# Performance work log

Hardware: AMD Instinct MI355X
Metric: run time of the kernel (lower is better)

Reference implementation:

```python
import jax, jax.numpy as jnp
import numpy as np

N_WORD, N_TOPIC, N_DOC = 50000, 2000, 50000
D_WORD, D_TOPIC, D_OUT = 256, 128, 128
E_WW, E_WT, E_WD, E_TD, E_TT = 500000, 400000, 500000, 400000, 300000


def setup_inputs() -> dict:
    key = jax.random.key(0)
    ks = jax.random.split(key, 32)
    i = iter(range(32))

    def randn(shape, scale=1.0):
        return jax.random.normal(ks[next(i)], shape, dtype=jnp.float32) * scale

    def edges(n_e, n_src, n_dst):
        src = jax.random.randint(ks[next(i)], (n_e,), 0, n_src, dtype=jnp.int32)
        dst = jax.random.randint(ks[next(i)], (n_e,), 0, n_dst, dtype=jnp.int32)
        w = jax.random.uniform(ks[next(i)], (n_e,), dtype=jnp.float32)
        return src, dst, w

    feat_word = randn((N_WORD, D_WORD))
    feat_topic = randn((N_TOPIC, D_TOPIC))
    ww_src, ww_dst, ww_w = edges(E_WW, N_WORD, N_WORD)
    wt_src, wt_dst, wt_w = edges(E_WT, N_WORD, N_TOPIC)
    wd_src, wd_dst, wd_w = edges(E_WD, N_WORD, N_DOC)
    td_src, td_dst, td_w = edges(E_TD, N_TOPIC, N_DOC)
    tt_src, tt_dst, tt_w = edges(E_TT, N_TOPIC, N_TOPIC)
    return dict(
        feat_word=feat_word, feat_topic=feat_topic,
        ww_src=ww_src, ww_dst=ww_dst, ww_w=ww_w,
        wt_src=wt_src, wt_dst=wt_dst, wt_w=wt_w,
        wd_src=wd_src, wd_dst=wd_dst, wd_w=wd_w,
        td_src=td_src, td_dst=td_dst, td_w=td_w,
        tt_src=tt_src, tt_dst=tt_dst, tt_w=tt_w,
        W_ww=randn((D_WORD, D_OUT), 0.02), b_ww=randn((D_OUT,), 0.02),
        W_wt=randn((D_WORD, D_OUT), 0.02), b_wt=randn((D_OUT,), 0.02),
        W_wd=randn((D_WORD, D_OUT), 0.02), b_wd=randn((D_OUT,), 0.02),
        W_td=randn((D_TOPIC, D_OUT), 0.02), b_td=randn((D_OUT,), 0.02),
        W_tt=randn((D_TOPIC, D_OUT), 0.02), b_tt=randn((D_OUT,), 0.02),
    )


def _mean_agg(Wh, src, dst, w, n_dst):
    # u_mul_e: gather src feature, scale by edge weight; fn.mean: divide by in-degree
    m = Wh[src] * w[:, None]                                   # [E, D_OUT]
    s = jax.ops.segment_sum(m, dst, num_segments=n_dst)        # [n_dst, D_OUT]
    deg = jax.ops.segment_sum(jnp.ones_like(w), dst, num_segments=n_dst)
    return jnp.where(deg[:, None] > 0, s / jnp.maximum(deg, 1.0)[:, None], 0.0)


def reference(feat_word, feat_topic,
              ww_src, ww_dst, ww_w, wt_src, wt_dst, wt_w,
              wd_src, wd_dst, wd_w, td_src, td_dst, td_w,
              tt_src, tt_dst, tt_w,
              W_ww, b_ww, W_wt, b_wt, W_wd, b_wd, W_td, b_td, W_tt, b_tt):
    # Per-relation projections (note: in the torch source the causal/noise
    # branches are overwritten by the plain Linear, so this is the effective math).
    Wh_ww = feat_word @ W_ww + b_ww
    Wh_wt = feat_word @ W_wt + b_wt
    Wh_wd = feat_word @ W_wd + b_wd
    Wh_td = feat_topic @ W_td + b_td
    Wh_tt = feat_topic @ W_tt + b_tt
    # mean per edge type, then cross-etype 'sum' per destination node type
    h_word = _mean_agg(Wh_ww, ww_src, ww_dst, ww_w, N_WORD)
    h_topic = (_mean_agg(Wh_wt, wt_src, wt_dst, wt_w, N_TOPIC)
               + _mean_agg(Wh_tt, tt_src, tt_dst, tt_w, N_TOPIC))
    h_doc = (_mean_agg(Wh_wd, wd_src, wd_dst, wd_w, N_DOC)
             + _mean_agg(Wh_td, td_src, td_dst, td_w, N_DOC))
    return h_word, h_topic, h_doc
```

## Files before the change

### kernel.cpp

```cpp
#include <hip/hip_runtime.h>

typedef short short8 __attribute__((ext_vector_type(8)));
typedef float floatx4 __attribute__((ext_vector_type(4)));

__device__ __forceinline__ float b2f(unsigned int u16) {
    union { unsigned int i; float f; } v;
    v.i = u16 << 16;
    return v.f;
}
__device__ __forceinline__ unsigned short f2b(float f) {
    unsigned int i = __float_as_uint(f);
    unsigned int r = (i + 0x7FFFu + ((i >> 16) & 1u)) >> 16;
    return (unsigned short)r;
}

#define N_WORD  50000
#define N_TOPIC 2000
#define N_DOC   50000
#define E_MAX   500000
#define CHAIN_END 0xFFFFFFFFu
#define NB_GEMM 814
#define NSLOT_WW 200000
#define NSLOT_WT 8000
#define NSLOT_TT 8000
#define NSLOT_WD 200000
#define NSLOT_TD 200000
#define NSLOT_ALL (NSLOT_WW + NSLOT_WT + NSLOT_TT + NSLOT_WD + NSLOT_TD)

__global__ void detect_kernel(const unsigned int* __restrict__ feat_u32,
                              unsigned int* __restrict__ flag)
{
    int cnt = 0;
    for (int i = 0; i < 256; ++i) {
        unsigned int u = feat_u32[i];
        int e = (u >> 7) & 0xFF;
        if (e >= 110 && e <= 140) ++cnt;
    }
    *flag = (cnt > 128) ? 1u : 0u;
}

__global__ __launch_bounds__(256) void swizzle_kernel(
    const void* __restrict__ W0, const void* __restrict__ W1,
    const void* __restrict__ W2, const void* __restrict__ W3,
    const void* __restrict__ W4,
    const void* __restrict__ b0, const void* __restrict__ b1,
    const void* __restrict__ b2, const void* __restrict__ b3,
    const void* __restrict__ b4,
    short8* __restrict__ D0, short8* __restrict__ D1,
    short8* __restrict__ D2, short8* __restrict__ D3,
    short8* __restrict__ D4,
    unsigned short* __restrict__ bias_out,
    const unsigned int* __restrict__ flag_p)
{
    const int w = blockIdx.y;
    const void* W; const void* bs; short8* D; int S;
    switch (w) {
        case 0: W = W0; bs = b0; D = D0; S = 8; break;
        case 1: W = W1; bs = b1; D = D1; S = 8; break;
        case 2: W = W2; bs = b2; D = D2; S = 8; break;
        case 3: W = W3; bs = b3; D = D3; S = 4; break;
        default: W = W4; bs = b4; D = D4; S = 4; break;
    }
    const int n_entries = S * 8 * 64;
    const int mode = (int)*flag_p;
    for (int e = blockIdx.x * 256 + threadIdx.x; e < n_entries; e += 8 * 256) {
        const int lane = e & 63, t = (e >> 6) & 7, s = e >> 9;
        const int q = lane >> 4, n = t * 16 + (lane & 15);
        short8 val;
#pragma unroll
        for (int j = 0; j < 8; ++j) {
            const int k = s * 32 + q * 8 + j;
            unsigned short hv = mode ? ((const unsigned short*)W)[k * 128 + n]
                                     : f2b(((const float*)W)[k * 128 + n]);
            val[j] = (short)hv;
        }
        D[e] = val;
    }
    if (blockIdx.x == 0 && threadIdx.x < 128) {
        bias_out[w * 128 + threadIdx.x] =
            mode ? ((const unsigned short*)bs)[threadIdx.x]
                 : f2b(((const float*)bs)[threadIdx.x]);
    }
}

template <int S, int NP>
__device__ __forceinline__ void gemm_body_lds(
    short8* __restrict__ Blds,
    const void* feat_, int n_rows, int bx,
    const short8* Ba, const short8* Bb, const short8* Bc,
    const unsigned short* bias_all, int ba, int bb, int bc,
    unsigned short* Oa, unsigned short* Ob, unsigned short* Oc,
    int mode_bf16)
{
    const int tid = threadIdx.x;
    const int lane = tid & 63;
    const int wave = tid >> 6;
    const int row0 = (bx * 4 + wave) * 16;
    const int m = lane & 15, q = lane >> 4;
    const int K = S * 32;
    int arow_idx = row0 + m;
    if (arow_idx >= n_rows) arow_idx = n_rows - 1;

    short8 a[S];
    if (mode_bf16) {
        const short8* arow = (const short8*)((const unsigned short*)feat_ + (size_t)arow_idx * K);
#pragma unroll
        for (int s = 0; s < S; ++s) a[s] = arow[s * 4 + q];
    } else {
        const float* arow = (const float*)feat_ + (size_t)arow_idx * K;
#pragma unroll
        for (int s = 0; s < S; ++s) {
            const float4 f0 = ((const float4*)arow)[s * 8 + q * 2];
            const float4 f1 = ((const float4*)arow)[s * 8 + q * 2 + 1];
            short8 t;
            t[0] = (short)f2b(f0.x); t[1] = (short)f2b(f0.y);
            t[2] = (short)f2b(f0.z); t[3] = (short)f2b(f0.w);
            t[4] = (short)f2b(f1.x); t[5] = (short)f2b(f1.y);
            t[6] = (short)f2b(f1.z); t[7] = (short)f2b(f1.w);
            a[s] = t;
        }
    }

    constexpr int NH = (S * 8 * 64 > 2048) ? 2 : 1;
    constexpr int SH = S / NH;

#pragma unroll
    for (int p = 0; p < NP; ++p) {
        const short8* B = (p == 0) ? Ba : ((p == 1) ? Bb : Bc);
        const unsigned short* bias = bias_all + ((p == 0) ? ba : ((p == 1) ? bb : bc)) * 128;
        unsigned short* O = (p == 0) ? Oa : ((p == 1) ? Ob : Oc);

        floatx4 acc[8];
#pragma unroll
        for (int t = 0; t < 8; ++t) { acc[t][0] = 0.f; acc[t][1] = 0.f; acc[t][2] = 0.f; acc[t][3] = 0.f; }

#pragma unroll
        for (int h = 0; h < NH; ++h) {
            __syncthreads();
            for (int i = tid; i < SH * 8 * 64; i += 256) Blds[i] = B[h * (SH * 8 * 64) + i];
            __syncthreads();
#pragma unroll
            for (int s = 0; s < SH; ++s) {
#pragma unroll
                for (int t = 0; t < 8; ++t) {
                    short8 b = Blds[(s * 8 + t) * 64 + lane];
                    acc[t] = __builtin_amdgcn_mfma_f32_16x16x32_bf16(a[h * SH + s], b, acc[t], 0, 0, 0);
                }
            }
        }

#pragma unroll
        for (int t = 0; t < 8; ++t) {
            const float bb_ = b2f((unsigned int)bias[t * 16 + m]);
#pragma unroll
            for (int r = 0; r < 4; ++r) {
                const int row = row0 + q * 4 + r;
                if (row < n_rows)
                    O[(size_t)row * 128 + t * 16 + m] = f2b(acc[t][r] + bb_);
            }
        }
    }
}

__global__ __launch_bounds__(256) void link_gemm_kernel(
    const void* __restrict__ feat_word, const void* __restrict__ feat_topic,
    const short8* __restrict__ Bww, const short8* __restrict__ Bwt,
    const short8* __restrict__ Bwd, const short8* __restrict__ Btt,
    const short8* __restrict__ Btd,
    const unsigned short* __restrict__ bias_all,
    unsigned short* __restrict__ Wh_ww, unsigned short* __restrict__ Wh_wt,
    unsigned short* __restrict__ Wh_wd, unsigned short* __restrict__ Wh_tt,
    unsigned short* __restrict__ Wh_td,
    const int* s0, const int* d0, const void* w0, int n0, unsigned int* h0, unsigned long long* e0,
    const int* s1, const int* d1, const void* w1, int n1, unsigned int* h1, unsigned long long* e1,
    const int* s2, const int* d2, const void* w2, int n2, unsigned int* h2, unsigned long long* e2,
    const int* s3, const int* d3, const void* w3, int n3, unsigned int* h3, unsigned long long* e3,
    const int* s4, const int* d4, const void* w4, int n4, unsigned int* h4, unsigned long long* e4,
    const unsigned int* __restrict__ flag_p)
{
    __shared__ short8 Blds[2048];
    const int mode = (int)*flag_p;

    if (blockIdx.x < NB_GEMM) {
        if (blockIdx.x < 782) {
            gemm_body_lds<8, 3>(Blds, feat_word, N_WORD, blockIdx.x, Bww, Bwt, Bwd,
                                bias_all, 0, 1, 2, Wh_ww, Wh_wt, Wh_wd, mode);
        } else {
            gemm_body_lds<4, 2>(Blds, feat_topic, N_TOPIC, blockIdx.x - 782, Btt, Btd,
                                (const short8*)nullptr, bias_all, 4, 3, 0,
                                Wh_tt, Wh_td, (unsigned short*)nullptr, mode);
        }
        return;
    }

    int lb = blockIdx.x - NB_GEMM;
    const int nb0 = (n0 + 255) >> 8, nb1 = (n1 + 255) >> 8, nb2 = (n2 + 255) >> 8,
              nb3 = (n3 + 255) >> 8;
    const int* src; const int* dst; const void* w_; int n;
    unsigned int* head; unsigned long long* ent;
    if (lb < nb0)      { src = s0; dst = d0; w_ = w0; n = n0; head = h0; ent = e0; }
    else if ((lb -= nb0) < nb1) { src = s1; dst = d1; w_ = w1; n = n1; head = h1; ent = e1; }
    else if ((lb -= nb1) < nb2) { src = s2; dst = d2; w_ = w2; n = n2; head = h2; ent = e2; }
    else if ((lb -= nb2) < nb3) { src = s3; dst = d3; w_ = w3; n = n3; head = h3; ent = e3; }
    else { lb -= nb3;  src = s4; dst = d4; w_ = w4; n = n4; head = h4; ent = e4; }

    const int i = lb * 256 + threadIdx.x;
    if (i >= n) return;
    const int d = dst[i];
    const unsigned int slot = (unsigned int)d * 4 + ((unsigned int)i & 3);
    const unsigned int old = atomicExch(&head[slot], (unsigned int)i);
    const unsigned short w16 = mode ? ((const unsigned short*)w_)[i]
                                    : f2b(((const float*)w_)[i]);
    ent[i] = ((unsigned long long)old << 32)
           | ((unsigned long long)w16 << 16)
           | (unsigned long long)(unsigned int)src[i];
}

__device__ __forceinline__ void acc8(float a[8], const uint4& u, float w)
{
    a[0] += b2f(u.x & 0xffffu) * w; a[1] += b2f(u.x >> 16) * w;
    a[2] += b2f(u.y & 0xffffu) * w; a[3] += b2f(u.y >> 16) * w;
    a[4] += b2f(u.z & 0xffffu) * w; a[5] += b2f(u.z >> 16) * w;
    a[6] += b2f(u.w & 0xffffu) * w; a[7] += b2f(u.w >> 16) * w;
}

__device__ __forceinline__ void walk1(
    const unsigned long long* __restrict__ ent,
    const unsigned short* __restrict__ Wh,
    unsigned int e, int sl, float a[8], float& cnt)
{
    bool live = (e != CHAIN_END);
    unsigned long long v = ent[live ? e : 0];
    while (live) {
        const unsigned int nx = (unsigned int)(v >> 32);
        const bool live_n = (nx != CHAIN_END);
        const unsigned long long vn = ent[live_n ? nx : 0];
        const uint4 u = ((const uint4*)(Wh + (size_t)((unsigned int)v & 0xffffu) * 128))[sl];
        acc8(a, u, b2f(((unsigned int)v) >> 16));
        cnt += 1.0f;
        v = vn; live = live_n;
    }
}

__device__ __forceinline__ void walk2(
    const unsigned long long* __restrict__ ent1, const unsigned short* __restrict__ Wh1, unsigned int e1,
    const unsigned long long* __restrict__ ent2, const unsigned short* __restrict__ Wh2, unsigned int e2,
    int sl, float a1[8], float a2[8], float& c1, float& c2)
{
    bool l1 = (e1 != CHAIN_END), l2 = (e2 != CHAIN_END);
    unsigned long long v1 = ent1[l1 ? e1 : 0];
    unsigned long long v2 = ent2[l2 ? e2 : 0];
    while (l1 || l2) {
        const unsigned int n1 = (unsigned int)(v1 >> 32);
        const unsigned int n2 = (unsigned int)(v2 >> 32);
        const bool l1n = l1 && (n1 != CHAIN_END);
        const bool l2n = l2 && (n2 != CHAIN_END);
        const unsigned long long v1n = ent1[l1n ? n1 : 0];
        const unsigned long long v2n = ent2[l2n ? n2 : 0];
        const uint4 u1 = ((const uint4*)(Wh1 + (size_t)((unsigned int)v1 & 0xffffu) * 128))[sl];
        const uint4 u2 = ((const uint4*)(Wh2 + (size_t)((unsigned int)v2 & 0xffffu) * 128))[sl];
        if (l1) { acc8(a1, u1, b2f(((unsigned int)v1) >> 16)); c1 += 1.0f; }
        if (l2) { acc8(a2, u2, b2f(((unsigned int)v2) >> 16)); c2 += 1.0f; }
        v1 = v1n; v2 = v2n; l1 = l1n; l2 = l2n;
    }
}

__device__ __forceinline__ void write8(
    void* out, size_t off_elems, int node, int sl, const float r[8], int mode)
{
    if (mode) {
        uint4 o;
        o.x = (unsigned int)f2b(r[0]) | ((unsigned int)f2b(r[1]) << 16);
        o.y = (unsigned int)f2b(r[2]) | ((unsigned int)f2b(r[3]) << 16);
        o.z = (unsigned int)f2b(r[4]) | ((unsigned int)f2b(r[5]) << 16);
        o.w = (unsigned int)f2b(r[6]) | ((unsigned int)f2b(r[7]) << 16);
        *(uint4*)((unsigned short*)out + off_elems + (size_t)node * 128 + sl * 8) = o;
    } else {
        float* p = (float*)out + off_elems + (size_t)node * 128 + sl * 8;
        ((float4*)p)[0] = make_float4(r[0], r[1], r[2], r[3]);
        ((float4*)p)[1] = make_float4(r[4], r[5], r[6], r[7]);
    }
}

__device__ __forceinline__ void dual_body(
    const unsigned int* __restrict__ h1, const unsigned long long* __restrict__ e1t,
    const unsigned short* __restrict__ Wh1,
    const unsigned int* __restrict__ h2, const unsigned long long* __restrict__ e2t,
    const unsigned short* __restrict__ Wh2,
    void* __restrict__ out, size_t off_elems, int blk, int mode)
{
    const int sl = threadIdx.x & 15;
    const int grp = (threadIdx.x >> 4) & 3;
    const int wave = threadIdx.x >> 6;
    const int node = blk * 4 + wave;
    float a1[8] = {0,0,0,0,0,0,0,0}, a2[8] = {0,0,0,0,0,0,0,0};
    float c1 = 0.f, c2 = 0.f;
    walk2(e1t, Wh1, h1[node * 4 + grp], e2t, Wh2, h2[node * 4 + grp],
          sl, a1, a2, c1, c2);
#pragma unroll
    for (int j = 0; j < 8; ++j) {
        a1[j] += __shfl_xor(a1[j], 16); a1[j] += __shfl_xor(a1[j], 32);
        a2[j] += __shfl_xor(a2[j], 16); a2[j] += __shfl_xor(a2[j], 32);
    }
    c1 += __shfl_xor(c1, 16); c1 += __shfl_xor(c1, 32);
    c2 += __shfl_xor(c2, 16); c2 += __shfl_xor(c2, 32);
    const float i1 = (c1 > 0.f) ? 1.f / c1 : 0.f;
    const float i2 = (c2 > 0.f) ? 1.f / c2 : 0.f;
    float r[8];
#pragma unroll
    for (int j = 0; j < 8; ++j) r[j] = a1[j] * i1 + a2[j] * i2;
    if (grp == 0) write8(out, off_elems, node, sl, r, mode);
}

__device__ __forceinline__ void word_body(
    const unsigned int* __restrict__ h_ww, const unsigned long long* __restrict__ e_ww,
    const unsigned short* __restrict__ Wh_ww,
    void* __restrict__ out, int blk, int mode)
{
    const int sl = threadIdx.x & 15;
    const int grp = (threadIdx.x >> 4) & 3;
    const int wave = threadIdx.x >> 6;
    const int node = blk * 4 + wave;
    float a[8] = {0,0,0,0,0,0,0,0}; float cnt = 0.f;
    walk1(e_ww, Wh_ww, h_ww[node * 4 + grp], sl, a, cnt);
#pragma unroll
    for (int j = 0; j < 8; ++j) { a[j] += __shfl_xor(a[j], 16); a[j] += __shfl_xor(a[j], 32); }
    cnt += __shfl_xor(cnt, 16); cnt += __shfl_xor(cnt, 32);
    const float inv = (cnt > 0.f) ? 1.f / cnt : 0.f;
    float r[8];
#pragma unroll
    for (int j = 0; j < 8; ++j) r[j] = a[j] * inv;
    if (grp == 0) write8(out, 0, node, sl, r, mode);
}

__global__ __launch_bounds__(256) void gather_all_kernel(
    const unsigned int* __restrict__ h_wt, const unsigned long long* __restrict__ e_wt,
    const unsigned short* __restrict__ Wh_wt,
    const unsigned int* __restrict__ h_tt, const unsigned long long* __restrict__ e_tt,
    const unsigned short* __restrict__ Wh_tt,
    const unsigned int* __restrict__ h_wd, const unsigned long long* __restrict__ e_wd,
    const unsigned short* __restrict__ Wh_wd,
    const unsigned int* __restrict__ h_td, const unsigned long long* __restrict__ e_td,
    const unsigned short* __restrict__ Wh_td,
    const unsigned int* __restrict__ h_ww, const unsigned long long* __restrict__ e_ww,
    const unsigned short* __restrict__ Wh_ww,
    void* __restrict__ out,
    const unsigned int* __restrict__ flag_p)
{
    const int mode = (int)*flag_p;
    if (blockIdx.x < 500) {
        dual_body(h_wt, e_wt, Wh_wt, h_tt, e_tt, Wh_tt,
                  out, (size_t)6400000, blockIdx.x, mode);
    } else if (blockIdx.x < 13000) {
        dual_body(h_wd, e_wd, Wh_wd, h_td, e_td, Wh_td,
                  out, (size_t)6656000, blockIdx.x - 500, mode);
    } else {
        word_body(h_ww, e_ww, Wh_ww, out, blockIdx.x - 13000, mode);
    }
}

__global__ __launch_bounds__(256) void gather_dt_kernel(
    const unsigned int* __restrict__ h_wt, const unsigned long long* __restrict__ e_wt,
    const unsigned short* __restrict__ Wh_wt,
    const unsigned int* __restrict__ h_tt, const unsigned long long* __restrict__ e_tt,
    const unsigned short* __restrict__ Wh_tt,
    const unsigned int* __restrict__ h_wd, const unsigned long long* __restrict__ e_wd,
    const unsigned short* __restrict__ Wh_wd,
    const unsigned int* __restrict__ h_td, const unsigned long long* __restrict__ e_td,
    const unsigned short* __restrict__ Wh_td,
    void* __restrict__ out,
    const unsigned int* __restrict__ flag_p)
{
    const int mode = (int)*flag_p;
    if (blockIdx.x < 500) {
        dual_body(h_wt, e_wt, Wh_wt, h_tt, e_tt, Wh_tt,
                  out, (size_t)6400000, blockIdx.x, mode);
    } else {
        dual_body(h_wd, e_wd, Wh_wd, h_td, e_td, Wh_td,
                  out, (size_t)6656000, blockIdx.x - 500, mode);
    }
}

__global__ __launch_bounds__(256) void gather_w_kernel(
    const unsigned int* __restrict__ h_ww, const unsigned long long* __restrict__ e_ww,
    const unsigned short* __restrict__ Wh_ww,
    void* __restrict__ out,
    const unsigned int* __restrict__ flag_p)
{
    word_body(h_ww, e_ww, Wh_ww, out, blockIdx.x, (int)*flag_p);
}

extern "C" void kernel_launch(void* const* d_in, const int* in_sizes, int n_in,
                              void* d_out, int out_size, void* d_ws, size_t ws_size,
                              hipStream_t stream)
{
    const void* feat_word  = d_in[0];
    const void* feat_topic = d_in[1];
    const int* ww_src = (const int*)d_in[2];
    const int* ww_dst = (const int*)d_in[3];
    const void* ww_w = d_in[4];
    const int* wt_src = (const int*)d_in[5];
    const int* wt_dst = (const int*)d_in[6];
    const void* wt_w = d_in[7];
    const int* wd_src = (const int*)d_in[8];
    const int* wd_dst = (const int*)d_in[9];
    const void* wd_w = d_in[10];
    const int* td_src = (const int*)d_in[11];
    const int* td_dst = (const int*)d_in[12];
    const void* td_w = d_in[13];
    const int* tt_src = (const int*)d_in[14];
    const int* tt_dst = (const int*)d_in[15];
    const void* tt_w = d_in[16];
    const void* W_ww = d_in[17];
    const void* b_ww = d_in[18];
    const void* W_wt = d_in[19];
    const void* b_wt = d_in[20];
    const void* W_wd = d_in[21];
    const void* b_wd = d_in[22];
    const void* W_td = d_in[23];
    const void* b_td = d_in[24];
    const void* W_tt = d_in[25];
    const void* b_tt = d_in[26];

    const int E_ww = in_sizes[2];
    const int E_wt = in_sizes[5];
    const int E_wd = in_sizes[8];
    const int E_td = in_sizes[11];
    const int E_tt = in_sizes[14];

    char* ws = (char*)d_ws;
    unsigned int* flag = (unsigned int*)ws;
    unsigned int* head_base = (unsigned int*)(ws + 4);
    unsigned int* h_ww = head_base;
    unsigned int* h_wt = h_ww + NSLOT_WW;
    unsigned int* h_tt = h_wt + NSLOT_WT;
    unsigned int* h_wd = h_tt + NSLOT_TT;
    unsigned int* h_td = h_wd + NSLOT_WD;
    size_t off = 4 + (size_t)NSLOT_ALL * 4;
    off = (off + 15) & ~(size_t)15;
    short8* Bsw_ww = (short8*)(ws + off); off += 65536;
    short8* Bsw_wt = (short8*)(ws + off); off += 65536;
    short8* Bsw_wd = (short8*)(ws + off); off += 65536;
    short8* Bsw_td = (short8*)(ws + off); off += 32768;
    short8* Bsw_tt = (short8*)(ws + off); off += 32768;
    unsigned short* bias_all = (unsigned short*)(ws + off); off += 5 * 128 * 2;
    off = (off + 15) & ~(size_t)15;
    unsigned short* Wh_ww = (unsigned short*)(ws + off); off += (size_t)N_WORD * 128 * 2;
    unsigned short* Wh_wt = (unsigned short*)(ws + off); off += (size_t)N_WORD * 128 * 2;
    unsigned short* Wh_tt = (unsigned short*)(ws + off); off += (size_t)N_TOPIC * 128 * 2;
    unsigned short* Wh_td = (unsigned short*)(ws + off); off += (size_t)N_TOPIC * 128 * 2;
    off = (off + 7) & ~(size_t)7;
    unsigned long long* e_ww = (unsigned long long*)(ws + off); off += (size_t)E_MAX * 8;
    unsigned long long* e_wt = (unsigned long long*)(ws + off); off += (size_t)E_MAX * 8;
    unsigned long long* e_tt = (unsigned long long*)(ws + off); off += (size_t)E_MAX * 8;
    unsigned long long* e_wd = (unsigned long long*)(ws + off); off += (size_t)E_MAX * 8;
    unsigned long long* e_td = (unsigned long long*)(ws + off); off += (size_t)E_MAX * 8;

    off = (off + 15) & ~(size_t)15;
    const size_t whwd_bytes = (size_t)N_WORD * 128 * 2;
    const bool fuse_gather = (ws_size >= off + whwd_bytes);
    unsigned short* Wh_wd = fuse_gather ? (unsigned short*)(ws + off)
                                        : (unsigned short*)d_out;

    detect_kernel<<<1, 1, 0, stream>>>((const unsigned int*)feat_word, flag);
    hipMemsetAsync(head_base, 0xFF, (size_t)NSLOT_ALL * 4, stream);

    swizzle_kernel<<<dim3(8, 5), 256, 0, stream>>>(
        W_ww, W_wt, W_wd, W_td, W_tt, b_ww, b_wt, b_wd, b_td, b_tt,
        Bsw_ww, Bsw_wt, Bsw_wd, Bsw_td, Bsw_tt, bias_all, flag);

    const int nb_link = ((E_ww + 255) / 256) + ((E_wt + 255) / 256) +
                        ((E_tt + 255) / 256) + ((E_wd + 255) / 256) +
                        ((E_td + 255) / 256);
    link_gemm_kernel<<<NB_GEMM + nb_link, 256, 0, stream>>>(
        feat_word, feat_topic, Bsw_ww, Bsw_wt, Bsw_wd, Bsw_tt, Bsw_td,
        bias_all, Wh_ww, Wh_wt, Wh_wd, Wh_tt, Wh_td,
        ww_src, ww_dst, ww_w, E_ww, h_ww, e_ww,
        wt_src, wt_dst, wt_w, E_wt, h_wt, e_wt,
        tt_src, tt_dst, tt_w, E_tt, h_tt, e_tt,
        wd_src, wd_dst, wd_w, E_wd, h_wd, e_wd,
        td_src, td_dst, td_w, E_td, h_td, e_td, flag);

    if (fuse_gather) {
        gather_all_kernel<<<500 + 12500 + 12500, 256, 0, stream>>>(
            h_wt, e_wt, Wh_wt, h_tt, e_tt, Wh_tt,
            h_wd, e_wd, Wh_wd, h_td, e_td, Wh_td,
            h_ww, e_ww, Wh_ww, d_out, flag);
    } else {
        gather_dt_kernel<<<500 + 12500, 256, 0, stream>>>(
            h_wt, e_wt, Wh_wt, h_tt, e_tt, Wh_tt,
            h_wd, e_wd, Wh_wd, h_td, e_td, Wh_td, d_out, flag);
        gather_w_kernel<<<12500, 256, 0, stream>>>(
            h_ww, e_ww, Wh_ww, d_out, flag);
    }
}
```

Measured before the change: 381.1 us.

## Replace linked-list edge chains with per-destination fixed-capacity slabs plus overflow lists

For the word-word, word-doc and topic-doc relations, edges are now bucketed into per-destination slabs of capacity C using an atomic counter, with a linked-list overflow chain for nodes whose degree exceeds C. The gather kernels read payloads contiguously and issue up to four row loads at once, instead of chasing dependent pointers through 4-way split chains. Each node is now handled by a 16-lane group rather than a full wave. The aim is to cut the serial latency of pointer chasing in the gather. The trade-offs are contended atomicAdd on counters, slab capacity sized from leftover workspace, and always using the unfused two-kernel gather path with Wh_wd placed in the output buffer.

```diff
diff --git a/kernel.cpp b/kernel.cpp
--- a/kernel.cpp
+++ b/kernel.cpp
@@ -17,15 +17,11 @@
 #define N_WORD  50000
 #define N_TOPIC 2000
 #define N_DOC   50000
-#define E_MAX   500000
 #define CHAIN_END 0xFFFFFFFFu
 #define NB_GEMM 814
-#define NSLOT_WW 200000
-#define NSLOT_WT 8000
-#define NSLOT_TT 8000
-#define NSLOT_WD 200000
-#define NSLOT_TD 200000
-#define NSLOT_ALL (NSLOT_WW + NSLOT_WT + NSLOT_TT + NSLOT_WD + NSLOT_TD)
+#define NPAD    50048
+#define NSLOT_WT (N_TOPIC * 4)
+#define NSLOT_TT (N_TOPIC * 4)
 
 __global__ void detect_kernel(const unsigned int* __restrict__ feat_u32,
                               unsigned int* __restrict__ flag)
@@ -162,6 +158,26 @@
     }
 }
 
+__device__ __forceinline__ void link_slab(
+    const int* __restrict__ src, const int* __restrict__ dst,
+    const void* __restrict__ w_, int n, int i, int mode, int C,
+    unsigned int* __restrict__ cnt, unsigned int* __restrict__ ohead,
+    unsigned long long* __restrict__ oent, unsigned int* __restrict__ slab)
+{
+    if (i >= n) return;
+    const int d = dst[i];
+    const unsigned short w16 = mode ? ((const unsigned short*)w_)[i]
+                                    : f2b(((const float*)w_)[i]);
+    const unsigned int pay = ((unsigned int)w16 << 16) | (unsigned int)src[i];
+    const unsigned int pos = atomicAdd(&cnt[d], 1u);
+    if (pos < (unsigned int)C) {
+        slab[(size_t)d * C + pos] = pay;
+    } else {
+        const unsigned int old = atomicExch(&ohead[d], (unsigned int)i);
+        oent[i] = ((unsigned long long)old << 32) | (unsigned long long)pay;
+    }
+}
+
 __global__ __launch_bounds__(256) void link_gemm_kernel(
     const void* __restrict__ feat_word, const void* __restrict__ feat_topic,
     const short8* __restrict__ Bww, const short8* __restrict__ Bwt,
@@ -171,11 +187,15 @@
     unsigned short* __restrict__ Wh_ww, unsigned short* __restrict__ Wh_wt,
     unsigned short* __restrict__ Wh_wd, unsigned short* __restrict__ Wh_tt,
     unsigned short* __restrict__ Wh_td,
-    const int* s0, const int* d0, const void* w0, int n0, unsigned int* h0, unsigned long long* e0,
+    const int* s0, const int* d0, const void* w0, int n0,
+    unsigned int* cnt0, unsigned int* oh0, unsigned long long* oe0, unsigned int* sl0,
+    const int* s3, const int* d3, const void* w3, int n3,
+    unsigned int* cnt3, unsigned int* oh3, unsigned long long* oe3, unsigned int* sl3,
+    const int* s4, const int* d4, const void* w4, int n4,
+    unsigned int* cnt4, unsigned int* oh4, unsigned long long* oe4, unsigned int* sl4,
     const int* s1, const int* d1, const void* w1, int n1, unsigned int* h1, unsigned long long* e1,
     const int* s2, const int* d2, const void* w2, int n2, unsigned int* h2, unsigned long long* e2,
-    const int* s3, const int* d3, const void* w3, int n3, unsigned int* h3, unsigned long long* e3,
-    const int* s4, const int* d4, const void* w4, int n4, unsigned int* h4, unsigned long long* e4,
+    int C,
     const unsigned int* __restrict__ flag_p)
 {
     __shared__ short8 Blds[2048];
@@ -196,24 +216,43 @@
     int lb = blockIdx.x - NB_GEMM;
     const int nb0 = (n0 + 255) >> 8, nb1 = (n1 + 255) >> 8, nb2 = (n2 + 255) >> 8,
               nb3 = (n3 + 255) >> 8;
-    const int* src; const int* dst; const void* w_; int n;
-    unsigned int* head; unsigned long long* ent;
-    if (lb < nb0)      { src = s0; dst = d0; w_ = w0; n = n0; head = h0; ent = e0; }
-    else if ((lb -= nb0) < nb1) { src = s1; dst = d1; w_ = w1; n = n1; head = h1; ent = e1; }
-    else if ((lb -= nb1) < nb2) { src = s2; dst = d2; w_ = w2; n = n2; head = h2; ent = e2; }
-    else if ((lb -= nb2) < nb3) { src = s3; dst = d3; w_ = w3; n = n3; head = h3; ent = e3; }
-    else { lb -= nb3;  src = s4; dst = d4; w_ = w4; n = n4; head = h4; ent = e4; }
-
-    const int i = lb * 256 + threadIdx.x;
-    if (i >= n) return;
-    const int d = dst[i];
-    const unsigned int slot = (unsigned int)d * 4 + ((unsigned int)i & 3);
-    const unsigned int old = atomicExch(&head[slot], (unsigned int)i);
-    const unsigned short w16 = mode ? ((const unsigned short*)w_)[i]
-                                    : f2b(((const float*)w_)[i]);
-    ent[i] = ((unsigned long long)old << 32)
-           | ((unsigned long long)w16 << 16)
-           | (unsigned long long)(unsigned int)src[i];
+    if (lb < nb0) {
+        link_slab(s0, d0, w0, n0, lb * 256 + threadIdx.x, mode, C, cnt0, oh0, oe0, sl0);
+        return;
+    }
+    lb -= nb0;
+    if (lb < nb1) {
+        const int i = lb * 256 + threadIdx.x;
+        if (i >= n1) return;
+        const int d = d1[i];
+        const unsigned int slot = (unsigned int)d * 4 + ((unsigned int)i & 3);
+        const unsigned int old = atomicExch(&h1[slot], (unsigned int)i);
+        const unsigned short w16 = mode ? ((const unsigned short*)w1)[i]
+                                        : f2b(((const float*)w1)[i]);
+        e1[i] = ((unsigned long long)old << 32) | ((unsigned long long)w16 << 16)
+              | (unsigned long long)(unsigned int)s1[i];
+        return;
+    }
+    lb -= nb1;
+    if (lb < nb2) {
+        const int i = lb * 256 + threadIdx.x;
+        if (i >= n2) return;
+        const int d = d2[i];
+        const unsigned int slot = (unsigned int)d * 4 + ((unsigned int)i & 3);
+        const unsigned int old = atomicExch(&h2[slot], (unsigned int)i);
+        const unsigned short w16 = mode ? ((const unsigned short*)w2)[i]
+                                        : f2b(((const float*)w2)[i]);
+        e2[i] = ((unsigned long long)old << 32) | ((unsigned long long)w16 << 16)
+              | (unsigned long long)(unsigned int)s2[i];
+        return;
+    }
+    lb -= nb2;
+    if (lb < nb3) {
+        link_slab(s3, d3, w3, n3, lb * 256 + threadIdx.x, mode, C, cnt3, oh3, oe3, sl3);
+        return;
+    }
+    lb -= nb3;
+    link_slab(s4, d4, w4, n4, lb * 256 + threadIdx.x, mode, C, cnt4, oh4, oe4, sl4);
 }
 
 __device__ __forceinline__ void acc8(float a[8], const uint4& u, float w)
@@ -223,6 +262,32 @@
     a[4] += b2f(u.z & 0xffffu) * w; a[5] += b2f(u.z >> 16) * w;
     a[6] += b2f(u.w & 0xffffu) * w; a[7] += b2f(u.w >> 16) * w;
 }
+__device__ __forceinline__ uint4 rowld(const unsigned short* Wh, unsigned int pay, int sl)
+{
+    return ((const uint4*)(Wh + (size_t)(pay & 0xffffu) * 128))[sl];
+}
+
+__device__ __forceinline__ void run_slab(
+    const unsigned int* __restrict__ slab, size_t b, int k,
+    const unsigned short* __restrict__ Wh, int sl, float a[8])
+{
+    for (int j = 0; j < k; j += 4) {
+        const int m = k - j;
+        unsigned int e0 = slab[b + j], e1 = 0, e2 = 0, e3 = 0;
+        if (m > 1) e1 = slab[b + j + 1];
+        if (m > 2) e2 = slab[b + j + 2];
+        if (m > 3) e3 = slab[b + j + 3];
+        uint4 r0, r1, r2, r3;
+        r0 = rowld(Wh, e0, sl);
+        if (m > 1) r1 = rowld(Wh, e1, sl);
+        if (m > 2) r2 = rowld(Wh, e2, sl);
+        if (m > 3) r3 = rowld(Wh, e3, sl);
+        acc8(a, r0, b2f(e0 >> 16));
+        if (m > 1) acc8(a, r1, b2f(e1 >> 16));
+        if (m > 2) acc8(a, r2, b2f(e2 >> 16));
+        if (m > 3) acc8(a, r3, b2f(e3 >> 16));
+    }
+}
 
 __device__ __forceinline__ void walk1(
     const unsigned long long* __restrict__ ent,
@@ -230,12 +295,14 @@
     unsigned int e, int sl, float a[8], float& cnt)
 {
     bool live = (e != CHAIN_END);
-    unsigned long long v = ent[live ? e : 0];
+    unsigned long long v = 0;
+    if (live) v = ent[e];
     while (live) {
         const unsigned int nx = (unsigned int)(v >> 32);
         const bool live_n = (nx != CHAIN_END);
-        const unsigned long long vn = ent[live_n ? nx : 0];
-        const uint4 u = ((const uint4*)(Wh + (size_t)((unsigned int)v & 0xffffu) * 128))[sl];
+        unsigned long long vn = 0;
+        if (live_n) vn = ent[nx];
+        const uint4 u = rowld(Wh, (unsigned int)v, sl);
         acc8(a, u, b2f(((unsigned int)v) >> 16));
         cnt += 1.0f;
         v = vn; live = live_n;
@@ -248,17 +315,20 @@
     int sl, float a1[8], float a2[8], float& c1, float& c2)
 {
     bool l1 = (e1 != CHAIN_END), l2 = (e2 != CHAIN_END);
-    unsigned long long v1 = ent1[l1 ? e1 : 0];
-    unsigned long long v2 = ent2[l2 ? e2 : 0];
+    unsigned long long v1 = 0, v2 = 0;
+    if (l1) v1 = ent1[e1];
+    if (l2) v2 = ent2[e2];
     while (l1 || l2) {
         const unsigned int n1 = (unsigned int)(v1 >> 32);
         const unsigned int n2 = (unsigned int)(v2 >> 32);
         const bool l1n = l1 && (n1 != CHAIN_END);
         const bool l2n = l2 && (n2 != CHAIN_END);
-        const unsigned long long v1n = ent1[l1n ? n1 : 0];
-        const unsigned long long v2n = ent2[l2n ? n2 : 0];
-        const uint4 u1 = ((const uint4*)(Wh1 + (size_t)((unsigned int)v1 & 0xffffu) * 128))[sl];
-        const uint4 u2 = ((const uint4*)(Wh2 + (size_t)((unsigned int)v2 & 0xffffu) * 128))[sl];
+        unsigned long long v1n = 0, v2n = 0;
+        if (l1n) v1n = ent1[n1];
+        if (l2n) v2n = ent2[n2];
+        uint4 u1, u2;
+        if (l1) u1 = rowld(Wh1, (unsigned int)v1, sl);
+        if (l2) u2 = rowld(Wh2, (unsigned int)v2, sl);
         if (l1) { acc8(a1, u1, b2f(((unsigned int)v1) >> 16)); c1 += 1.0f; }
         if (l2) { acc8(a2, u2, b2f(((unsigned int)v2) >> 16)); c2 += 1.0f; }
         v1 = v1n; v2 = v2n; l1 = l1n; l2 = l2n;
@@ -282,7 +352,21 @@
     }
 }
 
-__device__ __forceinline__ void dual_body(
+__device__ __forceinline__ void slab_mean_acc(
+    const unsigned int* __restrict__ cnt, const unsigned int* __restrict__ ohead,
+    const unsigned long long* __restrict__ oent, const unsigned int* __restrict__ slab,
+    const unsigned short* __restrict__ Wh, int node, int C, int sl, float a[8], float& deg)
+{
+    const int c = (int)cnt[node];
+    deg = (float)c;
+    run_slab(slab, (size_t)node * C, (c < C) ? c : C, Wh, sl, a);
+    if (c > C) {
+        float dummy = 0.f;
+        walk1(oent, Wh, ohead[node], sl, a, dummy);
+    }
+}
+
+__device__ __forceinline__ void topic_body(
     const unsigned int* __restrict__ h1, const unsigned long long* __restrict__ e1t,
     const unsigned short* __restrict__ Wh1,
     const unsigned int* __restrict__ h2, const unsigned long long* __restrict__ e2t,
@@ -312,82 +396,60 @@
     if (grp == 0) write8(out, off_elems, node, sl, r, mode);
 }
 
-__device__ __forceinline__ void word_body(
-    const unsigned int* __restrict__ h_ww, const unsigned long long* __restrict__ e_ww,
-    const unsigned short* __restrict__ Wh_ww,
-    void* __restrict__ out, int blk, int mode)
-{
-    const int sl = threadIdx.x & 15;
-    const int grp = (threadIdx.x >> 4) & 3;
-    const int wave = threadIdx.x >> 6;
-    const int node = blk * 4 + wave;
-    float a[8] = {0,0,0,0,0,0,0,0}; float cnt = 0.f;
-    walk1(e_ww, Wh_ww, h_ww[node * 4 + grp], sl, a, cnt);
-#pragma unroll
-    for (int j = 0; j < 8; ++j) { a[j] += __shfl_xor(a[j], 16); a[j] += __shfl_xor(a[j], 32); }
-    cnt += __shfl_xor(cnt, 16); cnt += __shfl_xor(cnt, 32);
-    const float inv = (cnt > 0.f) ? 1.f / cnt : 0.f;
-    float r[8];
-#pragma unroll
-    for (int j = 0; j < 8; ++j) r[j] = a[j] * inv;
-    if (grp == 0) write8(out, 0, node, sl, r, mode);
-}
-
-__global__ __launch_bounds__(256) void gather_all_kernel(
-    const unsigned int* __restrict__ h_wt, const unsigned long long* __restrict__ e_wt,
-    const unsigned short* __restrict__ Wh_wt,
-    const unsigned int* __restrict__ h_tt, const unsigned long long* __restrict__ e_tt,
-    const unsigned short* __restrict__ Wh_tt,
-    const unsigned int* __restrict__ h_wd, const unsigned long long* __restrict__ e_wd,
-    const unsigned short* __restrict__ Wh_wd,
-    const unsigned int* __restrict__ h_td, const unsigned long long* __restrict__ e_td,
-    const unsigned short* __restrict__ Wh_td,
-    const unsigned int* __restrict__ h_ww, const unsigned long long* __restrict__ e_ww,
-    const unsigned short* __restrict__ Wh_ww,
-    void* __restrict__ out,
-    const unsigned int* __restrict__ flag_p)
-{
-    const int mode = (int)*flag_p;
-    if (blockIdx.x < 500) {
-        dual_body(h_wt, e_wt, Wh_wt, h_tt, e_tt, Wh_tt,
-                  out, (size_t)6400000, blockIdx.x, mode);
-    } else if (blockIdx.x < 13000) {
-        dual_body(h_wd, e_wd, Wh_wd, h_td, e_td, Wh_td,
-                  out, (size_t)6656000, blockIdx.x - 500, mode);
-    } else {
-        word_body(h_ww, e_ww, Wh_ww, out, blockIdx.x - 13000, mode);
-    }
-}
-
 __global__ __launch_bounds__(256) void gather_dt_kernel(
     const unsigned int* __restrict__ h_wt, const unsigned long long* __restrict__ e_wt,
     const unsigned short* __restrict__ Wh_wt,
     const unsigned int* __restrict__ h_tt, const unsigned long long* __restrict__ e_tt,
     const unsigned short* __restrict__ Wh_tt,
-    const unsigned int* __restrict__ h_wd, const unsigned long long* __restrict__ e_wd,
+    const unsigned int* __restrict__ cnt_wd, const unsigned int* __restrict__ oh_wd,
+    const unsigned long long* __restrict__ oe_wd, const unsigned int* __restrict__ sl_wd,
     const unsigned short* __restrict__ Wh_wd,
-    const unsigned int* __restrict__ h_td, const unsigned long long* __restrict__ e_td,
+    const unsigned int* __restrict__ cnt_td, const unsigned int* __restrict__ oh_td,
+    const unsigned long long* __restrict__ oe_td, const unsigned int* __restrict__ sl_td,
     const unsigned short* __restrict__ Wh_td,
+    int C,
     void* __restrict__ out,
     const unsigned int* __restrict__ flag_p)
 {
     const int mode = (int)*flag_p;
     if (blockIdx.x < 500) {
-        dual_body(h_wt, e_wt, Wh_wt, h_tt, e_tt, Wh_tt,
-                  out, (size_t)6400000, blockIdx.x, mode);
+        topic_body(h_wt, e_wt, Wh_wt, h_tt, e_tt, Wh_tt,
+                   out, (size_t)6400000, blockIdx.x, mode);
     } else {
-        dual_body(h_wd, e_wd, Wh_wd, h_td, e_td, Wh_td,
-                  out, (size_t)6656000, blockIdx.x - 500, mode);
+        const int sl = threadIdx.x & 15;
+        const int node = (blockIdx.x - 500) * 16 + (threadIdx.x >> 4);
+        float a1[8] = {0,0,0,0,0,0,0,0}, a2[8] = {0,0,0,0,0,0,0,0};
+        float dg1, dg2;
+        slab_mean_acc(cnt_wd, oh_wd, oe_wd, sl_wd, Wh_wd, node, C, sl, a1, dg1);
+        slab_mean_acc(cnt_td, oh_td, oe_td, sl_td, Wh_td, node, C, sl, a2, dg2);
+        const float i1 = (dg1 > 0.f) ? 1.f / dg1 : 0.f;
+        const float i2 = (dg2 > 0.f) ? 1.f / dg2 : 0.f;
+        float r[8];
+#pragma unroll
+        for (int j = 0; j < 8; ++j) r[j] = a1[j] * i1 + a2[j] * i2;
+        write8(out, (size_t)6656000, node, sl, r, mode);
     }
 }
 
 __global__ __launch_bounds__(256) void gather_w_kernel(
-    const unsigned int* __restrict__ h_ww, const unsigned long long* __restrict__ e_ww,
+    const unsigned int* __restrict__ cnt_ww, const unsigned int* __restrict__ oh_ww,
+    const unsigned long long* __restrict__ oe_ww, const unsigned int* __restrict__ sl_ww,
     const unsigned short* __restrict__ Wh_ww,
+    int C,
     void* __restrict__ out,
     const unsigned int* __restrict__ flag_p)
 {
-    word_body(h_ww, e_ww, Wh_ww, out, blockIdx.x, (int)*flag_p);
+    const int mode = (int)*flag_p;
+    const int sl = threadIdx.x & 15;
+    const int node = blockIdx.x * 16 + (threadIdx.x >> 4);
+    float a[8] = {0,0,0,0,0,0,0,0};
+    float dg;
+    slab_mean_acc(cnt_ww, oh_ww, oe_ww, sl_ww, Wh_ww, node, C, sl, a, dg);
+    const float inv = (dg > 0.f) ? 1.f / dg : 0.f;
+    float r[8];
+#pragma unroll
+    for (int j = 0; j < 8; ++j) r[j] = a[j] * inv;
+    write8(out, 0, node, sl, r, mode);
 }
 
 extern "C" void kernel_launch(void* const* d_in, const int* in_sizes, int n_in,
@@ -430,13 +492,19 @@
 
     char* ws = (char*)d_ws;
     unsigned int* flag = (unsigned int*)ws;
-    unsigned int* head_base = (unsigned int*)(ws + 4);
-    unsigned int* h_ww = head_base;
-    unsigned int* h_wt = h_ww + NSLOT_WW;
-    unsigned int* h_tt = h_wt + NSLOT_WT;
-    unsigned int* h_wd = h_tt + NSLOT_TT;
-    unsigned int* h_td = h_wd + NSLOT_WD;
-    size_t off = 4 + (size_t)NSLOT_ALL * 4;
+    size_t off = 16;
+    unsigned int* cnt_ww = (unsigned int*)(ws + off);
+    unsigned int* cnt_wd = cnt_ww + NPAD;
+    unsigned int* cnt_td = cnt_wd + NPAD;
+    const size_t cnt_bytes = (size_t)3 * NPAD * 4;
+    off += cnt_bytes;
+    unsigned int* oh_ww = (unsigned int*)(ws + off);
+    unsigned int* oh_wd = oh_ww + NPAD;
+    unsigned int* oh_td = oh_wd + NPAD;
+    unsigned int* h_wt  = oh_td + NPAD;
+    unsigned int* h_tt  = h_wt + NSLOT_WT;
+    const size_t ff_bytes = (size_t)3 * NPAD * 4 + (size_t)(NSLOT_WT + NSLOT_TT) * 4;
+    off += ff_bytes;
     off = (off + 15) & ~(size_t)15;
     short8* Bsw_ww = (short8*)(ws + off); off += 65536;
     short8* Bsw_wt = (short8*)(ws + off); off += 65536;
@@ -450,20 +518,26 @@
     unsigned short* Wh_tt = (unsigned short*)(ws + off); off += (size_t)N_TOPIC * 128 * 2;
     unsigned short* Wh_td = (unsigned short*)(ws + off); off += (size_t)N_TOPIC * 128 * 2;
     off = (off + 7) & ~(size_t)7;
-    unsigned long long* e_ww = (unsigned long long*)(ws + off); off += (size_t)E_MAX * 8;
-    unsigned long long* e_wt = (unsigned long long*)(ws + off); off += (size_t)E_MAX * 8;
-    unsigned long long* e_tt = (unsigned long long*)(ws + off); off += (size_t)E_MAX * 8;
-    unsigned long long* e_wd = (unsigned long long*)(ws + off); off += (size_t)E_MAX * 8;
-    unsigned long long* e_td = (unsigned long long*)(ws + off); off += (size_t)E_MAX * 8;
-
+    unsigned long long* oe_ww = (unsigned long long*)(ws + off); off += (size_t)E_ww * 8;
+    unsigned long long* oe_wd = (unsigned long long*)(ws + off); off += (size_t)E_wd * 8;
+    unsigned long long* oe_td = (unsigned long long*)(ws + off); off += (size_t)E_td * 8;
+    unsigned long long* e_wt  = (unsigned long long*)(ws + off); off += (size_t)E_wt * 8;
+    unsigned long long* e_tt  = (unsigned long long*)(ws + off); off += (size_t)E_tt * 8;
     off = (off + 15) & ~(size_t)15;
-    const size_t whwd_bytes = (size_t)N_WORD * 128 * 2;
-    const bool fuse_gather = (ws_size >= off + whwd_bytes);
-    unsigned short* Wh_wd = fuse_gather ? (unsigned short*)(ws + off)
-                                        : (unsigned short*)d_out;
+
+    size_t slab_budget = (ws_size > off) ? (ws_size - off) : 0;
+    int C = (int)(slab_budget / ((size_t)3 * N_WORD * 4));
+    if (C > 24) C = 24;
+    if (C < 2) C = 2;
+    unsigned int* sl_ww = (unsigned int*)(ws + off); off += (size_t)N_WORD * C * 4;
+    unsigned int* sl_wd = (unsigned int*)(ws + off); off += (size_t)N_DOC * C * 4;
+    unsigned int* sl_td = (unsigned int*)(ws + off); off += (size_t)N_DOC * C * 4;
+
+    unsigned short* Wh_wd = (unsigned short*)d_out;
 
     detect_kernel<<<1, 1, 0, stream>>>((const unsigned int*)feat_word, flag);
-    hipMemsetAsync(head_base, 0xFF, (size_t)NSLOT_ALL * 4, stream);
+    hipMemsetAsync(cnt_ww, 0x00, cnt_bytes, stream);
+    hipMemsetAsync(oh_ww, 0xFF, ff_bytes, stream);
 
     swizzle_kernel<<<dim3(8, 5), 256, 0, stream>>>(
         W_ww, W_wt, W_wd, W_td, W_tt, b_ww, b_wt, b_wd, b_td, b_tt,
@@ -475,22 +549,19 @@
     link_gemm_kernel<<<NB_GEMM + nb_link, 256, 0, stream>>>(
         feat_word, feat_topic, Bsw_ww, Bsw_wt, Bsw_wd, Bsw_tt, Bsw_td,
         bias_all, Wh_ww, Wh_wt, Wh_wd, Wh_tt, Wh_td,
-        ww_src, ww_dst, ww_w, E_ww, h_ww, e_ww,
+        ww_src, ww_dst, ww_w, E_ww, cnt_ww, oh_ww, oe_ww, sl_ww,
+        wd_src, wd_dst, wd_w, E_wd, cnt_wd, oh_wd, oe_wd, sl_wd,
+        td_src, td_dst, td_w, E_td, cnt_td, oh_td, oe_td, sl_td,
         wt_src, wt_dst, wt_w, E_wt, h_wt, e_wt,
         tt_src, tt_dst, tt_w, E_tt, h_tt, e_tt,
-        wd_src, wd_dst, wd_w, E_wd, h_wd, e_wd,
-        td_src, td_dst, td_w, E_td, h_td, e_td, flag);
-
-    if (fuse_gather) {
-        gather_all_kernel<<<500 + 12500 + 12500, 256, 0, stream>>>(
-            h_wt, e_wt, Wh_wt, h_tt, e_tt, Wh_tt,
-            h_wd, e_wd, Wh_wd, h_td, e_td, Wh_td,
-            h_ww, e_ww, Wh_ww, d_out, flag);
-    } else {
-        gather_dt_kernel<<<500 + 12500, 256, 0, stream>>>(
-            h_wt, e_wt, Wh_wt, h_tt, e_tt, Wh_tt,
-            h_wd, e_wd, Wh_wd, h_td, e_td, Wh_td, d_out, flag);
-        gather_w_kernel<<<12500, 256, 0, stream>>>(
-            h_ww, e_ww, Wh_ww, d_out, flag);
-    }
-}
+        C, flag);
+
+    gather_dt_kernel<<<500 + 3125, 256, 0, stream>>>(
+        h_wt, e_wt, Wh_wt, h_tt, e_tt, Wh_tt,
+        cnt_wd, oh_wd, oe_wd, sl_wd, Wh_wd,
+        cnt_td, oh_td, oe_td, sl_td, Wh_td,
+        C, d_out, flag);
+
+    gather_w_kernel<<<3125, 256, 0, stream>>>(
+        cnt_ww, oh_ww, oe_ww, sl_ww, Wh_ww, C, d_out, flag);
+}
```

Result: slower. 391.7 us (+2.8%).
